# Kernel optimization log

Hardware: AMD Instinct MI355X
Metric: run time of the kernel (lower is better)

The kernel has to match this reference:

```python
import jax, jax.numpy as jnp
import numpy as np

B, N, D, H, I = 16, 1024, 1024, 16, 4096
HS = D // H  # 64
EPS = 1e-5


def setup_inputs() -> dict:
    key = jax.random.key(0)
    ks = jax.random.split(key, 8)
    w = lambda k, shape: (jax.random.normal(k, shape, jnp.float32) * 0.02)
    return {
        'hidden_states': jax.random.normal(ks[0], (B, N, D), jnp.float32),
        'ln1_g': jnp.ones((D,), jnp.float32), 'ln1_b': jnp.zeros((D,), jnp.float32),
        'ln2_g': jnp.ones((D,), jnp.float32), 'ln2_b': jnp.zeros((D,), jnp.float32),
        'wq': w(ks[1], (D, D)), 'bq': jnp.zeros((D,), jnp.float32),
        'wk': w(ks[2], (D, D)), 'bk': jnp.zeros((D,), jnp.float32),
        'wv': w(ks[3], (D, D)), 'bv': jnp.zeros((D,), jnp.float32),
        'w1': w(ks[4], (D, I)), 'b1': jnp.zeros((I,), jnp.float32),
        'w2': w(ks[5], (I, D)), 'b2': jnp.zeros((D,), jnp.float32),
    }


def _layernorm(x, g, b):
    m = jnp.mean(x, axis=-1, keepdims=True)
    v = jnp.var(x, axis=-1, keepdims=True)
    return (x - m) * jax.lax.rsqrt(v + EPS) * g + b


def _split_heads(t):
    # Faithful to transpose_for_scores: reshape (B,N,HS,H) -> (B,H,N,HS)
    # i.e. head h takes the strided feature slice t[..., h::H].
    b, n, _ = t.shape
    return t.reshape(b, n, HS, H).transpose(0, 3, 1, 2)


def _vit_layer(x, ln1_g, ln1_b, ln2_g, ln2_b, wq, bq, wk, bk, wv, bv, w1, b1, w2, b2):
    h = _layernorm(x, ln1_g, ln1_b)
    q = _split_heads(h @ wq + bq)  # [B,H,N,HS]
    k = _split_heads(h @ wk + bk)
    v = _split_heads(h @ wv + bv)
    scores = jax.nn.softmax(jnp.einsum('bhqd,bhkd->bhqk', q, k) / np.sqrt(HS).astype(np.float32), axis=-1)
    attn = jnp.einsum('bhqk,bhkd->bhqd', scores, v)          # [B,H,N,HS]
    attn = attn.transpose(0, 2, 1, 3).reshape(x.shape)       # head-major merge (as in source)
    x = x + attn
    h = _layernorm(x, ln2_g, ln2_b)
    mlp = jax.nn.silu(h @ w1 + b1) @ w2 + b2
    return x + mlp


def reference(hidden_states, ln1_g, ln1_b, ln2_g, ln2_b, wq, bq, wk, bk, wv, bv, w1, b1, w2, b2):
    return _vit_layer(hidden_states, ln1_g, ln1_b, ln2_g, ln2_b, wq, bq, wk, bk, wv, bv, w1, b1, w2, b2)
```

## Files before the change

kernel.cpp:

```cpp
#include <hip/hip_runtime.h>
#include <hip/hip_bf16.h>
#include <stdint.h>

typedef __bf16 bf16;
typedef bf16 bf16x8 __attribute__((ext_vector_type(8)));
typedef bf16 bf16x4 __attribute__((ext_vector_type(4)));
typedef float f32x4 __attribute__((ext_vector_type(4)));

static __device__ __forceinline__ f32x4 mfma16(bf16x8 a, bf16x8 b, f32x4 c) {
    return __builtin_amdgcn_mfma_f32_16x16x32_bf16(a, b, c, 0, 0, 0);
}

static __device__ __forceinline__ void gld16(const bf16* g, bf16* l) {
    __builtin_amdgcn_global_load_lds((const __attribute__((address_space(1))) void*)g,
                                     (__attribute__((address_space(3))) void*)l, 16, 0, 0);
}

static __device__ __forceinline__ uint32_t pkbf(float a, float b) {
    union { bf16 h[2]; uint32_t u; } u_;
    u_.h[0] = (bf16)a; u_.h[1] = (bf16)b;
    return u_.u;
}

static __device__ __forceinline__ void xcd_supertile(int gdx, int gdy,
                                                     int& bx, int& by) {
    const int orig = blockIdx.y * gdx + blockIdx.x;
    const int xcd = orig & 7;
    const int idx = orig >> 3;
    const int CBY = gdy >> 3;
    const int gx = (gdx >= 4) ? 4 : gdx;
    const int gy = (CBY >= 4) ? 4 : CBY;
    const int cells = gx * gy;
    const int st = idx / cells, off = idx % cells;
    const int nstx = gdx / gx;
    const int stx = st % nstx, sty = st / nstx;
    bx = stx * gx + off % gx;
    by = xcd * CBY + sty * gy + off / gx;
}

template <int PERM>
__global__ __launch_bounds__(256)
void tcast_kernel(const float* __restrict__ src, bf16* __restrict__ dst, int R, int C) {
    __shared__ float t[32][33];
    const int tx = threadIdx.x, ty = threadIdx.y;
    const int c0 = blockIdx.x * 32, r0 = blockIdx.y * 32;
#pragma unroll
    for (int j = 0; j < 4; ++j)
        t[ty + j * 8][tx] = src[(size_t)(r0 + ty + j * 8) * C + c0 + tx];
    __syncthreads();
#pragma unroll
    for (int j = 0; j < 4; ++j) {
        const int c = c0 + ty + j * 8;
        const int cp = PERM ? (((c & 15) << 6) | (c >> 4)) : c;
        dst[(size_t)cp * R + r0 + tx] = (bf16)t[tx][ty + j * 8];
    }
}

__global__ __launch_bounds__(256)
void bperm_kernel(const float* __restrict__ b0, const float* __restrict__ b1,
                  const float* __restrict__ b2, float* __restrict__ dst) {
    const int i = blockIdx.x * 256 + threadIdx.x;
    const int seg = i >> 10, c = i & 1023;
    const int src = ((c & 63) << 4) | (c >> 6);
    const float* b = (seg == 0) ? b0 : (seg == 1) ? b1 : b2;
    dst[i] = b[src];
}

__global__ __launch_bounds__(256)
void ln_kernel(const float* __restrict__ x, const float* __restrict__ gg,
               const float* __restrict__ bb, bf16* __restrict__ out) {
    __shared__ float red[8];
    const int row = blockIdx.x, tid = threadIdx.x;
    const int lane = tid & 63, wid = tid >> 6;
    const float4 v = ((const float4*)(x + (size_t)row * 1024))[tid];
    float s  = v.x + v.y + v.z + v.w;
    float s2 = v.x * v.x + v.y * v.y + v.z * v.z + v.w * v.w;
#pragma unroll
    for (int m = 1; m <= 32; m <<= 1) {
        s  += __shfl_xor(s,  m);
        s2 += __shfl_xor(s2, m);
    }
    if (lane == 0) { red[wid] = s; red[wid + 4] = s2; }
    __syncthreads();
    float ts  = red[0] + red[1] + red[2] + red[3];
    float ts2 = red[4] + red[5] + red[6] + red[7];
    float mean = ts * (1.f / 1024.f);
    float var  = ts2 * (1.f / 1024.f) - mean * mean;
    float rs   = rsqrtf(var + 1e-5f);
    const float4 gv = ((const float4*)gg)[tid];
    const float4 bv = ((const float4*)bb)[tid];
    bf16x4 o;
    o[0] = (bf16)((v.x - mean) * rs * gv.x + bv.x);
    o[1] = (bf16)((v.y - mean) * rs * gv.y + bv.y);
    o[2] = (bf16)((v.z - mean) * rs * gv.z + bv.z);
    o[3] = (bf16)((v.w - mean) * rs * gv.w + bv.w);
    *(bf16x4*)(out + (size_t)row * 1024 + tid * 4) = o;
}

template <int MODE>
__global__ __launch_bounds__(256)
void gemm_bt(const bf16* __restrict__ A, const bf16* __restrict__ Bt,
             int M, int N, int K,
             const float* __restrict__ bias_a,
             const float* __restrict__ resid, float* __restrict__ outF,
             bf16* __restrict__ oQ, bf16* __restrict__ oK, bf16* __restrict__ oV,
             bf16* __restrict__ oB) {
    __shared__ alignas(16) bf16 As[3][128 * 32];
    __shared__ alignas(16) bf16 Bs[3][128 * 32];
    const int tid = threadIdx.x;
    const int wid = tid >> 6, lane = tid & 63;
    const int li = lane & 15, g = lane >> 4;

    int bx, by;
    xcd_supertile(gridDim.x, gridDim.y, bx, by);
    const int row0 = by * 128, col0 = bx * 128;

    const int gsrc = ((tid & 3) ^ ((tid >> 3) & 3)) * 8;
    const bf16* gA0 = A + (size_t)(row0 + (tid >> 2)) * K + gsrc;
    const bf16* gA1 = A + (size_t)(row0 + 64 + (tid >> 2)) * K + gsrc;
    const bf16* gB0 = Bt + (size_t)(col0 + (tid >> 2)) * K + gsrc;
    const bf16* gB1 = Bt + (size_t)(col0 + 64 + (tid >> 2)) * K + gsrc;

    const int wr = wid >> 1, wc = wid & 1;
    f32x4 acc[4][4] = {};

    const int nt = K >> 5;
#pragma unroll
    for (int p = 0; p < 2; ++p) {
        const int kk = p << 5;
        gld16(gA0 + kk, &As[p][wid * 512]);
        gld16(gA1 + kk, &As[p][wid * 512 + 2048]);
        gld16(gB0 + kk, &Bs[p][wid * 512]);
        gld16(gB1 + kk, &Bs[p][wid * 512 + 2048]);
    }

    const int sa = (li >> 1) & 3;
    const int rdoff = (g ^ sa) * 8;

    int cur = 0;
    for (int t = 0; t < nt; ++t) {
        if (t + 2 < nt) {
            const int k2 = (t + 2) << 5;
            const int nb = (cur + 2) % 3;
            gld16(gA0 + k2, &As[nb][wid * 512]);
            gld16(gA1 + k2, &As[nb][wid * 512 + 2048]);
            gld16(gB0 + k2, &Bs[nb][wid * 512]);
            gld16(gB1 + k2, &Bs[nb][wid * 512 + 2048]);
            asm volatile("s_waitcnt vmcnt(8)" ::: "memory");
        } else if (t + 1 < nt) {
            asm volatile("s_waitcnt vmcnt(4)" ::: "memory");
        } else {
            asm volatile("s_waitcnt vmcnt(0)" ::: "memory");
        }
        __builtin_amdgcn_s_barrier();
        __builtin_amdgcn_sched_barrier(0);

        bf16x8 af[4], bg[4];
        const bf16* pa = &As[cur][(wr * 64 + li) * 32 + rdoff];
        const bf16* pb = &Bs[cur][(wc * 64 + li) * 32 + rdoff];
#pragma unroll
        for (int i = 0; i < 4; ++i) af[i] = *(const bf16x8*)(pa + i * 512);
#pragma unroll
        for (int j = 0; j < 4; ++j) bg[j] = *(const bf16x8*)(pb + j * 512);
#pragma unroll
        for (int i = 0; i < 4; ++i)
#pragma unroll
            for (int j = 0; j < 4; ++j)
                acc[i][j] = mfma16(af[i], bg[j], acc[i][j]);
        __builtin_amdgcn_sched_barrier(0);
        __builtin_amdgcn_s_barrier();
        cur = (cur + 1) % 3;
    }

    if (MODE == 0) {
        const int seg = col0 >> 10;
        const int h   = ((col0 & 1023) >> 6) + wc;
        const int bb  = row0 >> 10;
        const int n0  = (row0 & 1023) + wr * 64;
        float bias[4];
#pragma unroll
        for (int j = 0; j < 4; ++j) bias[j] = bias_a[col0 + wc * 64 + j * 16 + li];

        if (seg == 2) {
#pragma unroll
            for (int i = 0; i < 4; ++i)
#pragma unroll
                for (int j = 0; j < 4; ++j) {
                    const int d = j * 16 + li;
                    bf16x4 pv;
#pragma unroll
                    for (int r = 0; r < 4; ++r) pv[r] = (bf16)(acc[i][j][r] + bias[j]);
                    *(bf16x4*)(oV + ((size_t)(bb * 16 + h) * 64 + d) * 1024
                                   + n0 + i * 16 + g * 4) = pv;
                }
        } else {
            char* ep = (wid < 3) ? ((char*)&As[0][0] + wid * 8192)
                                 : ((char*)&Bs[0][0]);
            const float scale = (seg == 0) ? 0.125f : 1.0f;
            bf16* og = (seg == 0) ? oQ : oK;
#pragma unroll
            for (int i = 0; i < 4; ++i)
#pragma unroll
                for (int j = 0; j < 4; ++j)
#pragma unroll
                    for (int r = 0; r < 4; ++r) {
                        const int rr = i * 16 + g * 4 + r;
                        const int byte = (rr * 128 + (j * 16 + li) * 2) ^ ((rr & 7) << 4);
                        *(bf16*)(ep + byte) = (bf16)((acc[i][j][r] + bias[j]) * scale);
                    }
            bf16* gb = og + ((size_t)(bb * 16 + h) * 1024 + n0) * 64;
#pragma unroll
            for (int t = 0; t < 8; ++t) {
                const int rr = t * 8 + (lane >> 3);
                const int d0 = (lane & 7) * 8;
                const int byte = (rr * 128 + d0 * 2) ^ ((rr & 7) << 4);
                bf16x8 val = *(const bf16x8*)(ep + byte);
                *(bf16x8*)(gb + (size_t)rr * 64 + d0) = val;
            }
        }
    } else {
#pragma unroll
        for (int i = 0; i < 4; ++i) {
            const int row = row0 + wr * 64 + i * 16 + g * 4;
#pragma unroll
            for (int j = 0; j < 4; ++j) {
                const int col = col0 + wc * 64 + j * 16 + li;
                f32x4 v = acc[i][j];
                if (MODE == 1) {
                    const float bias = bias_a[col];
#pragma unroll
                    for (int r = 0; r < 4; ++r) {
                        float val = v[r] + bias;
                        val = val / (1.f + __expf(-val));
                        oB[(size_t)(row + r) * N + col] = (bf16)val;
                    }
                } else {
                    const float bias = bias_a[col];
#pragma unroll
                    for (int r = 0; r < 4; ++r) {
                        const size_t idx = (size_t)(row + r) * N + col;
                        outF[idx] = v[r] + bias + resid[idx];
                    }
                }
            }
        }
    }
}

template <int MODE>
__global__ __launch_bounds__(512, 2)
void gemm256(const bf16* __restrict__ A, const bf16* __restrict__ Bt,
             int M, int N, int K,
             const float* __restrict__ bias_a,
             const float* __restrict__ resid, float* __restrict__ outF,
             bf16* __restrict__ oB) {
    __shared__ alignas(16) bf16 As[2][256 * 64];
    __shared__ alignas(16) bf16 Bs[2][256 * 64];
    const int tid = threadIdx.x;
    const int wid = tid >> 6, lane = tid & 63;
    const int li = lane & 15, g = lane >> 4;
    const int wm = wid >> 2, wn = wid & 3;

    int bx, by;
    xcd_supertile(gridDim.x, gridDim.y, bx, by);
    const int row0 = by * 256, col0 = bx * 256;

    const int gsrc = ((tid & 7) ^ ((tid >> 3) & 7)) << 3;
    const bf16* gA = A + (size_t)(row0 + (tid >> 3)) * K + gsrc;
    const bf16* gB = Bt + (size_t)(col0 + (tid >> 3)) * K + gsrc;

    f32x4 acc[8][4] = {};
    const int nt = K >> 6;

#pragma unroll
    for (int j = 0; j < 4; ++j) {
        gld16(gA + (size_t)(64 * j) * K, &As[0][j * 4096 + (wid << 9)]);
        gld16(gB + (size_t)(64 * j) * K, &Bs[0][j * 4096 + (wid << 9)]);
    }
    asm volatile("s_waitcnt vmcnt(0)" ::: "memory");
    __builtin_amdgcn_s_barrier();

    int cur = 0;
    for (int t = 0; t < nt; ++t) {
        const bf16* At = &As[cur][0];
        const bf16* Bl = &Bs[cur][0];
        bf16* Asn = &As[cur ^ 1][0];
        bf16* Bsn = &Bs[cur ^ 1][0];
        const bool pf = (t + 1 < nt);
        const size_t koff = (size_t)(t + 1) << 6;
        bf16x8 bfr[4][2];

#pragma unroll
        for (int p = 0; p < 4; ++p) {
            bf16x8 af[2][2];
#pragma unroll
            for (int ii = 0; ii < 2; ++ii) {
                const int rr = wm * 128 + (p * 2 + ii) * 16 + li;
#pragma unroll
                for (int ks = 0; ks < 2; ++ks)
                    af[ii][ks] = *(const bf16x8*)(At + rr * 64 + (((ks * 4 + g) ^ (li & 7)) << 3));
            }
            if (p == 0) {
#pragma unroll
                for (int jf = 0; jf < 4; ++jf) {
                    const int rb = wn * 64 + jf * 16 + li;
#pragma unroll
                    for (int ks = 0; ks < 2; ++ks)
                        bfr[jf][ks] = *(const bf16x8*)(Bl + rb * 64 + (((ks * 4 + g) ^ (li & 7)) << 3));
                }
            }
            if (pf) {
                if (p == 0) {
                    gld16(gB + koff,                     Bsn + (wid << 9));
                    gld16(gB + (size_t)64 * K + koff,    Bsn + 4096 + (wid << 9));
                } else if (p == 1) {
                    gld16(gB + (size_t)128 * K + koff,   Bsn + 2 * 4096 + (wid << 9));
                    gld16(gB + (size_t)192 * K + koff,   Bsn + 3 * 4096 + (wid << 9));
                } else if (p == 2) {
                    gld16(gA + koff,                     Asn + (wid << 9));
                    gld16(gA + (size_t)128 * K + koff,   Asn + 2 * 4096 + (wid << 9));
                } else {
                    gld16(gA + (size_t)64 * K + koff,    Asn + 4096 + (wid << 9));
                    gld16(gA + (size_t)192 * K + koff,   Asn + 3 * 4096 + (wid << 9));
                }
            }
            __builtin_amdgcn_s_barrier();
            asm volatile("s_waitcnt lgkmcnt(0)" ::: "memory");
            __builtin_amdgcn_sched_barrier(0);
            __builtin_amdgcn_s_setprio(1);
#pragma unroll
            for (int ii = 0; ii < 2; ++ii)
#pragma unroll
                for (int jf = 0; jf < 4; ++jf)
#pragma unroll
                    for (int ks = 0; ks < 2; ++ks)
                        acc[p * 2 + ii][jf] = mfma16(af[ii][ks], bfr[jf][ks], acc[p * 2 + ii][jf]);
            __builtin_amdgcn_s_setprio(0);
            __builtin_amdgcn_sched_barrier(0);
            if (p == 1) {
                if (pf) asm volatile("s_waitcnt vmcnt(4)" ::: "memory");
                else    asm volatile("s_waitcnt vmcnt(0)" ::: "memory");
            }
            if (p == 3 && pf)
                asm volatile("s_waitcnt vmcnt(2)" ::: "memory");
            __builtin_amdgcn_s_barrier();
        }
        cur ^= 1;
    }

#pragma unroll
    for (int i = 0; i < 8; ++i) {
        const int row = row0 + wm * 128 + i * 16 + g * 4;
#pragma unroll
        for (int jf = 0; jf < 4; ++jf) {
            const int col = col0 + wn * 64 + jf * 16 + li;
            const float bias = bias_a[col];
            if (MODE == 1) {
#pragma unroll
                for (int r = 0; r < 4; ++r) {
                    float val = acc[i][jf][r] + bias;
                    val = val / (1.f + __expf(-val));
                    oB[(size_t)(row + r) * N + col] = (bf16)val;
                }
            } else {
#pragma unroll
                for (int r = 0; r < 4; ++r) {
                    const size_t idx = (size_t)(row + r) * N + col;
                    outF[idx] = acc[i][jf][r] + bias + resid[idx];
                }
            }
        }
    }
}

__global__ __launch_bounds__(256)
void attn_kernel(const bf16* __restrict__ Q, const bf16* __restrict__ Kb,
                 const bf16* __restrict__ Vt, const float* __restrict__ x,
                 float* __restrict__ out) {
    __shared__ alignas(16) bf16 Kl[2][4096];
    __shared__ alignas(16) bf16 Vl[2][4096];
    __shared__ alignas(16) char Ps[4][4096];
    const int tid = threadIdx.x, wid = tid >> 6, lane = tid & 63;
    const int li = lane & 15, g = lane >> 4;
    const int bid = blockIdx.x;
    const int bh = (bid & 7) + ((bid >> 6) << 3);
    const int qt = (bid >> 3) & 7;
    const int b = bh >> 4, h = bh & 15;
    const size_t base = (size_t)bh << 16;
    const bf16* Qp = Q + base + (size_t)(qt * 128 + wid * 32) * 64;
    const bf16* Kp = Kb + base;
    const bf16* Vp = Vt + base;
    char* psw = Ps[wid];
    const int swz = (li & 7) << 4;

    const int srow = lane >> 3;
    const int sslot = (lane & 7) ^ srow;

    bf16x8 aq[2][2];
#pragma unroll
    for (int fr = 0; fr < 2; ++fr)
#pragma unroll
        for (int ks = 0; ks < 2; ++ks)
            aq[fr][ks] = *(const bf16x8*)(Qp + (fr * 16 + li) * 64 + ks * 32 + g * 8);

#pragma unroll
    for (int hh = 0; hh < 2; ++hh) {
        const int r = wid * 16 + hh * 8 + srow;
        gld16(Kp + (size_t)r * 64 + sslot * 8, &Kl[0][(wid * 16 + hh * 8) * 64]);
        gld16(Vp + (size_t)r * 1024 + sslot * 8, &Vl[0][(wid * 16 + hh * 8) * 64]);
    }
    asm volatile("s_waitcnt vmcnt(0)" ::: "memory");
    __builtin_amdgcn_s_barrier();

    f32x4 o[2][4] = {};
    float mrun[2] = {-1e30f, -1e30f}, lrun[2] = {0.f, 0.f};

    for (int kt = 0; kt < 16; ++kt) {
        const int cur = kt & 1;
        const bf16* Kt = Kl[cur];
        const bf16* Vtl = Vl[cur];
        if (kt < 15) {
            const int nb = (kt + 1) * 64;
#pragma unroll
            for (int hh = 0; hh < 2; ++hh) {
                const int r = wid * 16 + hh * 8 + srow;
                gld16(Kp + (size_t)(nb + r) * 64 + sslot * 8,
                      &Kl[cur ^ 1][(wid * 16 + hh * 8) * 64]);
                gld16(Vp + (size_t)r * 1024 + nb + sslot * 8,
                      &Vl[cur ^ 1][(wid * 16 + hh * 8) * 64]);
            }
            asm volatile("s_waitcnt vmcnt(4)" ::: "memory");
        } else {
            asm volatile("s_waitcnt vmcnt(0)" ::: "memory");
        }
        __builtin_amdgcn_s_barrier();
        __builtin_amdgcn_sched_barrier(0);

        f32x4 s[2][4] = {};
        __builtin_amdgcn_s_setprio(1);
#pragma unroll
        for (int jc = 0; jc < 4; ++jc) {
            const int row = jc * 16 + li;
#pragma unroll
            for (int ks = 0; ks < 2; ++ks) {
                bf16x8 kf = *(const bf16x8*)(Kt + row * 64 + (((ks * 4 + g) ^ (li & 7)) * 8));
                s[0][jc] = mfma16(kf, aq[0][ks], s[0][jc]);
                s[1][jc] = mfma16(kf, aq[1][ks], s[1][jc]);
            }
        }
        __builtin_amdgcn_s_setprio(0);

#pragma unroll
        for (int fr = 0; fr < 2; ++fr) {
            float mj[4];
#pragma unroll
            for (int jc = 0; jc < 4; ++jc)
                mj[jc] = fmaxf(fmaxf(s[fr][jc][0], s[fr][jc][1]),
                               fmaxf(s[fr][jc][2], s[fr][jc][3]));
            float mx = fmaxf(fmaxf(mj[0], mj[1]), fmaxf(mj[2], mj[3]));
            mx = fmaxf(mx, __shfl_xor(mx, 16));
            mx = fmaxf(mx, __shfl_xor(mx, 32));
            if (!__all(mx <= mrun[fr] + 8.f)) {
                const float mnew = fmaxf(mrun[fr], mx);
                const float alpha = __expf(mrun[fr] - mnew);
                mrun[fr] = mnew;
                lrun[fr] *= alpha;
#pragma unroll
                for (int jd = 0; jd < 4; ++jd) o[fr][jd] *= alpha;
            }
            float pj[4];
#pragma unroll
            for (int jc = 0; jc < 4; ++jc) {
#pragma unroll
                for (int r = 0; r < 4; ++r)
                    s[fr][jc][r] = __expf(s[fr][jc][r] - mrun[fr]);
                pj[jc] = (s[fr][jc][0] + s[fr][jc][1]) + (s[fr][jc][2] + s[fr][jc][3]);
            }
            float ps = (pj[0] + pj[1]) + (pj[2] + pj[3]);
            ps += __shfl_xor(ps, 16);
            ps += __shfl_xor(ps, 32);
            lrun[fr] += ps;

            const int qb = (fr * 16 + li) * 128;
#pragma unroll
            for (int jc = 0; jc < 4; ++jc) {
                uint2 w;
                w.x = pkbf(s[fr][jc][0], s[fr][jc][1]);
                w.y = pkbf(s[fr][jc][2], s[fr][jc][3]);
                *(uint2*)(psw + ((qb + jc * 32 + g * 8) ^ swz)) = w;
            }
        }

#pragma unroll
        for (int ks2 = 0; ks2 < 2; ++ks2) {
            bf16x8 pa0 = *(const bf16x8*)(psw + ((li * 128 + ks2 * 64 + g * 16) ^ swz));
            bf16x8 pa1 = *(const bf16x8*)(psw + (((16 + li) * 128 + ks2 * 64 + g * 16) ^ swz));
            __builtin_amdgcn_s_setprio(1);
#pragma unroll
            for (int jd = 0; jd < 4; ++jd) {
                const int row = jd * 16 + li;
                bf16x8 vf = *(const bf16x8*)(Vtl + row * 64 + (((ks2 * 4 + g) ^ (li & 7)) * 8));
                o[0][jd] = mfma16(vf, pa0, o[0][jd]);
                o[1][jd] = mfma16(vf, pa1, o[1][jd]);
            }
            __builtin_amdgcn_s_setprio(0);
        }
        __builtin_amdgcn_sched_barrier(0);
        __builtin_amdgcn_s_barrier();
    }

    const int n0 = qt * 128 + wid * 32;
#pragma unroll
    for (int fr = 0; fr < 2; ++fr) {
        const float inv = 1.f / lrun[fr];
        const int n = n0 + fr * 16 + li;
        const size_t rowb = (size_t)(b * 1024 + n) * 1024 + h * 64;
#pragma unroll
        for (int jd = 0; jd < 4; ++jd) {
            const int c = jd * 16 + g * 4;
            const float4 xv = *(const float4*)(x + rowb + c);
            float4 ov;
            ov.x = xv.x + o[fr][jd][0] * inv;
            ov.y = xv.y + o[fr][jd][1] * inv;
            ov.z = xv.z + o[fr][jd][2] * inv;
            ov.w = xv.w + o[fr][jd][3] * inv;
            *(float4*)(out + rowb + c) = ov;
        }
    }
}

extern "C" void kernel_launch(void* const* d_in, const int* in_sizes, int n_in,
                              void* d_out, int out_size, void* d_ws, size_t ws_size,
                              hipStream_t stream) {
    const float* x    = (const float*)d_in[0];
    const float* ln1g = (const float*)d_in[1];
    const float* ln1b = (const float*)d_in[2];
    const float* ln2g = (const float*)d_in[3];
    const float* ln2b = (const float*)d_in[4];
    const float* wq   = (const float*)d_in[5];
    const float* bq   = (const float*)d_in[6];
    const float* wk   = (const float*)d_in[7];
    const float* bk   = (const float*)d_in[8];
    const float* wv   = (const float*)d_in[9];
    const float* bv   = (const float*)d_in[10];
    const float* w1   = (const float*)d_in[11];
    const float* b1   = (const float*)d_in[12];
    const float* w2   = (const float*)d_in[13];
    const float* b2   = (const float*)d_in[14];

    char* ws = (char*)d_ws;
    const size_t MB = 1024 * 1024;
    bf16*  Wqkvt = (bf16*)(ws);
    bf16*  W1t   = (bf16*)(ws + 6 * MB);
    bf16*  W2t   = (bf16*)(ws + 14 * MB);
    float* ares  = (float*)(ws + 22 * MB);
    bf16*  Xln   = (bf16*)(ws + 86 * MB);
    bf16*  Qb    = (bf16*)(ws + 118 * MB);
    bf16*  Kbuf  = (bf16*)(ws + 150 * MB);
    bf16*  Vtb   = (bf16*)(ws + 182 * MB);
    bf16*  mid   = (bf16*)(ws + 118 * MB);
    float* bqkvp = (float*)(ws + 245 * MB);

    dim3 tb(32, 8);
    tcast_kernel<1><<<dim3(32, 32), tb, 0, stream>>>(wq, Wqkvt,                 1024, 1024);
    tcast_kernel<1><<<dim3(32, 32), tb, 0, stream>>>(wk, Wqkvt + 1024 * 1024,   1024, 1024);
    tcast_kernel<1><<<dim3(32, 32), tb, 0, stream>>>(wv, Wqkvt + 2 * 1024 * 1024, 1024, 1024);
    tcast_kernel<0><<<dim3(128, 32), tb, 0, stream>>>(w1, W1t, 1024, 4096);
    tcast_kernel<0><<<dim3(32, 128), tb, 0, stream>>>(w2, W2t, 4096, 1024);
    bperm_kernel<<<12, 256, 0, stream>>>(bq, bk, bv, bqkvp);

    ln_kernel<<<16384, 256, 0, stream>>>(x, ln1g, ln1b, Xln);

    gemm_bt<0><<<dim3(24, 128), 256, 0, stream>>>(Xln, Wqkvt, 16384, 3072, 1024,
        bqkvp, nullptr, nullptr, Qb, Kbuf, Vtb, nullptr);

    attn_kernel<<<2048, 256, 0, stream>>>(Qb, Kbuf, Vtb, x, ares);

    ln_kernel<<<16384, 256, 0, stream>>>(ares, ln2g, ln2b, Xln);

    gemm256<1><<<dim3(16, 64), 512, 0, stream>>>(Xln, W1t, 16384, 4096, 1024,
        b1, nullptr, nullptr, mid);

    gemm256<2><<<dim3(4, 64), 512, 0, stream>>>(mid, W2t, 16384, 1024, 4096,
        b2, ares, (float*)d_out, nullptr);
}
```

Measured before the change: 671.7 us.

## Restructure GEMM main loop with one barrier per k-tile and register-double-buffered A fragments

Reworks the 256x256 bf16 GEMM inner loop. It replaces the four barriers per phase with a single vmcnt(0) wait and barrier at the top of each k-tile. A fragments are ping-ponged between two register sets, with partial lgkmcnt waits so the next LDS reads overlap the current MFMAs. Global-to-LDS prefetches of B and then A are grouped into two bursts. This cuts synchronisation overhead and exposes more LDS latency hiding, at the cost of more live registers and a full global-load drain before each tile.

```diff
diff --git a/kernel.cpp b/kernel.cpp
--- a/kernel.cpp
+++ b/kernel.cpp
@@ -271,82 +271,96 @@
 
     f32x4 acc[8][4] = {};
     const int nt = K >> 6;
+    const int rdo0 = ((0 ^ (li & 7)) << 3) | ((4 ^ (li & 7)) << 3) * 0;
+
+    const int ro0 = (((0 * 4 + g) ^ (li & 7)) << 3);
+    const int ro1 = (((1 * 4 + g) ^ (li & 7)) << 3);
 
 #pragma unroll
     for (int j = 0; j < 4; ++j) {
         gld16(gA + (size_t)(64 * j) * K, &As[0][j * 4096 + (wid << 9)]);
         gld16(gB + (size_t)(64 * j) * K, &Bs[0][j * 4096 + (wid << 9)]);
     }
-    asm volatile("s_waitcnt vmcnt(0)" ::: "memory");
-    __builtin_amdgcn_s_barrier();
-
-    int cur = 0;
+
+#define RDA(dst, p)                                                        \
+    do {                                                                   \
+        _Pragma("unroll")                                                  \
+        for (int ii = 0; ii < 2; ++ii) {                                   \
+            const int rr = wm * 128 + ((p) * 2 + ii) * 16 + li;            \
+            dst[ii][0] = *(const bf16x8*)(At + rr * 64 + ro0);             \
+            dst[ii][1] = *(const bf16x8*)(At + rr * 64 + ro1);             \
+        }                                                                  \
+    } while (0)
+
+#define MFMAP(p, src)                                                      \
+    do {                                                                   \
+        __builtin_amdgcn_s_setprio(1);                                     \
+        _Pragma("unroll")                                                  \
+        for (int ii = 0; ii < 2; ++ii)                                     \
+            _Pragma("unroll")                                              \
+            for (int jf = 0; jf < 4; ++jf) {                               \
+                acc[(p) * 2 + ii][jf] = mfma16(src[ii][0], bfr[jf][0],     \
+                                               acc[(p) * 2 + ii][jf]);     \
+                acc[(p) * 2 + ii][jf] = mfma16(src[ii][1], bfr[jf][1],     \
+                                               acc[(p) * 2 + ii][jf]);     \
+            }                                                              \
+        __builtin_amdgcn_s_setprio(0);                                     \
+    } while (0)
+
     for (int t = 0; t < nt; ++t) {
-        const bf16* At = &As[cur][0];
-        const bf16* Bl = &Bs[cur][0];
-        bf16* Asn = &As[cur ^ 1][0];
-        bf16* Bsn = &Bs[cur ^ 1][0];
+        asm volatile("s_waitcnt vmcnt(0)" ::: "memory");
+        __builtin_amdgcn_s_barrier();
+        __builtin_amdgcn_sched_barrier(0);
+
+        const bf16* At = &As[t & 1][0];
+        const bf16* Bl = &Bs[t & 1][0];
+        bf16* Asn = &As[(t & 1) ^ 1][0];
+        bf16* Bsn = &Bs[(t & 1) ^ 1][0];
         const bool pf = (t + 1 < nt);
         const size_t koff = (size_t)(t + 1) << 6;
+
         bf16x8 bfr[4][2];
-
-#pragma unroll
-        for (int p = 0; p < 4; ++p) {
-            bf16x8 af[2][2];
-#pragma unroll
-            for (int ii = 0; ii < 2; ++ii) {
-                const int rr = wm * 128 + (p * 2 + ii) * 16 + li;
-#pragma unroll
-                for (int ks = 0; ks < 2; ++ks)
-                    af[ii][ks] = *(const bf16x8*)(At + rr * 64 + (((ks * 4 + g) ^ (li & 7)) << 3));
-            }
-            if (p == 0) {
-#pragma unroll
-                for (int jf = 0; jf < 4; ++jf) {
-                    const int rb = wn * 64 + jf * 16 + li;
-#pragma unroll
-                    for (int ks = 0; ks < 2; ++ks)
-                        bfr[jf][ks] = *(const bf16x8*)(Bl + rb * 64 + (((ks * 4 + g) ^ (li & 7)) << 3));
-                }
-            }
-            if (pf) {
-                if (p == 0) {
-                    gld16(gB + koff,                     Bsn + (wid << 9));
-                    gld16(gB + (size_t)64 * K + koff,    Bsn + 4096 + (wid << 9));
-                } else if (p == 1) {
-                    gld16(gB + (size_t)128 * K + koff,   Bsn + 2 * 4096 + (wid << 9));
-                    gld16(gB + (size_t)192 * K + koff,   Bsn + 3 * 4096 + (wid << 9));
-                } else if (p == 2) {
-                    gld16(gA + koff,                     Asn + (wid << 9));
-                    gld16(gA + (size_t)128 * K + koff,   Asn + 2 * 4096 + (wid << 9));
-                } else {
-                    gld16(gA + (size_t)64 * K + koff,    Asn + 4096 + (wid << 9));
-                    gld16(gA + (size_t)192 * K + koff,   Asn + 3 * 4096 + (wid << 9));
-                }
-            }
-            __builtin_amdgcn_s_barrier();
-            asm volatile("s_waitcnt lgkmcnt(0)" ::: "memory");
-            __builtin_amdgcn_sched_barrier(0);
-            __builtin_amdgcn_s_setprio(1);
-#pragma unroll
-            for (int ii = 0; ii < 2; ++ii)
-#pragma unroll
-                for (int jf = 0; jf < 4; ++jf)
-#pragma unroll
-                    for (int ks = 0; ks < 2; ++ks)
-                        acc[p * 2 + ii][jf] = mfma16(af[ii][ks], bfr[jf][ks], acc[p * 2 + ii][jf]);
-            __builtin_amdgcn_s_setprio(0);
-            __builtin_amdgcn_sched_barrier(0);
-            if (p == 1) {
-                if (pf) asm volatile("s_waitcnt vmcnt(4)" ::: "memory");
-                else    asm volatile("s_waitcnt vmcnt(0)" ::: "memory");
-            }
-            if (p == 3 && pf)
-                asm volatile("s_waitcnt vmcnt(2)" ::: "memory");
-            __builtin_amdgcn_s_barrier();
-        }
-        cur ^= 1;
-    }
+#pragma unroll
+        for (int jf = 0; jf < 4; ++jf) {
+            const int rb = wn * 64 + jf * 16 + li;
+            bfr[jf][0] = *(const bf16x8*)(Bl + rb * 64 + ro0);
+            bfr[jf][1] = *(const bf16x8*)(Bl + rb * 64 + ro1);
+        }
+        bf16x8 afA[2][2], afB[2][2];
+        RDA(afA, 0);
+        if (pf) {
+            gld16(gB + koff,                   Bsn + (wid << 9));
+            gld16(gB + (size_t)64 * K + koff,  Bsn + 4096 + (wid << 9));
+            gld16(gB + (size_t)128 * K + koff, Bsn + 2 * 4096 + (wid << 9));
+            gld16(gB + (size_t)192 * K + koff, Bsn + 3 * 4096 + (wid << 9));
+        }
+        RDA(afB, 1);
+        asm volatile("s_waitcnt lgkmcnt(4)" ::: "memory");
+        __builtin_amdgcn_sched_barrier(0);
+        MFMAP(0, afA);
+
+        RDA(afA, 2);
+        asm volatile("s_waitcnt lgkmcnt(4)" ::: "memory");
+        __builtin_amdgcn_sched_barrier(0);
+        MFMAP(1, afB);
+
+        if (pf) {
+            gld16(gA + koff,                   Asn + (wid << 9));
+            gld16(gA + (size_t)64 * K + koff,  Asn + 4096 + (wid << 9));
+            gld16(gA + (size_t)128 * K + koff, Asn + 2 * 4096 + (wid << 9));
+            gld16(gA + (size_t)192 * K + koff, Asn + 3 * 4096 + (wid << 9));
+        }
+        RDA(afB, 3);
+        asm volatile("s_waitcnt lgkmcnt(4)" ::: "memory");
+        __builtin_amdgcn_sched_barrier(0);
+        MFMAP(2, afA);
+
+        asm volatile("s_waitcnt lgkmcnt(0)" ::: "memory");
+        __builtin_amdgcn_sched_barrier(0);
+        MFMAP(3, afB);
+    }
+#undef RDA
+#undef MFMAP
 
 #pragma unroll
     for (int i = 0; i < 8; ++i) {
@@ -371,6 +385,7 @@
             }
         }
     }
+    (void)rdo0;
 }
 
 __global__ __launch_bounds__(256)
```

Measured after the change: 656.0 us. -2.3%, faster.
